# Kernel tuning notes

Measured on AMD Instinct MI355X. Metric: run time of the kernel, lower is better.

## Reference

```python
import jax, jax.numpy as jnp
import numpy as np

N_NODES = 50000
N_COLORS = 256
D = 64
H = 128  # MLP hidden = 2*D
E_VV = 800000
E_VC = 400000


def _mlp_params(key, d_in, d_hid, d_out):
    k1, k2 = jax.random.split(key)
    s1 = 1.0 / np.sqrt(d_in)
    s2 = 1.0 / np.sqrt(d_hid)
    return (
        jax.random.uniform(k1, (d_in, d_hid), jnp.float32, -s1, s1),
        jnp.zeros((d_hid,), jnp.float32),
        jax.random.uniform(k2, (d_hid, d_out), jnp.float32, -s2, s2),
        jnp.zeros((d_out,), jnp.float32),
    )


def setup_inputs() -> dict:
    key = jax.random.key(0)
    ks = jax.random.split(key, 8)
    x_v = jax.random.normal(ks[0], (N_NODES, D), jnp.float32)
    x_c = jax.random.normal(ks[1], (N_COLORS, D), jnp.float32)
    src_vv = jax.random.randint(ks[2], (E_VV,), 0, N_NODES, jnp.int32)
    dst_vv = jax.random.randint(ks[3], (E_VV,), 0, N_NODES, jnp.int32)
    src_vc = jax.random.randint(ks[4], (E_VC,), 0, N_COLORS, jnp.int32)
    dst_vc = jax.random.randint(ks[5], (E_VC,), 0, N_NODES, jnp.int32)
    W1v, b1v, W2v, b2v = _mlp_params(ks[6], D, H, D)
    W1c, b1c, W2c, b2c = _mlp_params(ks[7], D, H, D)
    return {
        "x_v": x_v, "x_c": x_c,
        "W1v": W1v, "b1v": b1v, "W2v": W2v, "b2v": b2v,
        "W1c": W1c, "b1c": b1c, "W2c": W2c, "b2c": b2c,
        "src_vv": src_vv, "dst_vv": dst_vv,
        "src_vc": src_vc, "dst_vc": dst_vc,
    }


def reference(x_v, x_c, W1v, b1v, W2v, b2v, W1c, b1c, W2c, b2c,
              src_vv, dst_vv, src_vc, dst_vc):
    n = x_v.shape[0]
    # vertex->vertex messages: gather, MLP, scatter-sum
    mv = jax.nn.relu(x_v[src_vv] @ W1v + b1v) @ W2v + b2v  # [E_vv, D]
    agg_v = jax.ops.segment_sum(mv, dst_vv, num_segments=n)
    # color->vertex messages: gather color embeddings, MLP, scatter-sum
    mc = jax.nn.relu(x_c[src_vc] @ W1c + b1c) @ W2c + b2c  # [E_vc, D]
    agg_c = jax.ops.segment_sum(mc, dst_vc, num_segments=n)
    return jax.nn.relu(x_v + agg_v + agg_c)
```

## Files before the change

kernel.cpp:

```cpp
#include <hip/hip_runtime.h>

#define NN 50000
#define NC 256
#define DD 64
#define HH 128
#define EVV 800000
#define EVC 400000
#define NE 1200000
#define NB 196
#define BCAP 8192
#define MLPV_B 782
#define MLPC_B 4
#define MLP_B (MLPV_B + MLPC_B)
#define FILL_EPB 2048
#define FILL_B 586
#define QUADS 197
#define K1_B (QUADS * 7)
#define VCAP 64
#define HROW 136

typedef __attribute__((ext_vector_type(8))) short bf16x8;
typedef __attribute__((ext_vector_type(4))) float f32x4;

__device__ __forceinline__ unsigned short f2bf(float x) {
  unsigned u = __float_as_uint(x);
  u = (u + 0x7fffu + ((u >> 16) & 1u)) >> 16;
  return (unsigned short)u;
}

union SMem {
  unsigned short hl[4][16 * HROW];
  struct {
    int cnt[NB];
    int off[NB];
    int gbase[NB];
    int sa[256], sb[256];
    unsigned int stage[FILL_EPB];
  } f;
};

__global__ __launch_bounds__(256) void prep_kernel(
    const float* __restrict__ W1v, const float* __restrict__ W2v,
    const float* __restrict__ W1c, const float* __restrict__ W2c,
    unsigned short* __restrict__ wt, int* __restrict__ gcur) {
  const int tid = blockIdx.x * 256 + threadIdx.x;
  if (tid < NB) gcur[tid] = 0;
  const int sel = tid >> 13;
  const int t = tid & 8191;
  unsigned short* dst = wt + sel * 8192;
  if (sel == 0) {
    const int n = t >> 6, k = t & 63;
    dst[t] = f2bf(W1v[k * HH + n]);
  } else if (sel == 1) {
    const int n = t >> 7, k = t & 127;
    dst[t] = f2bf(W2v[k * DD + n]);
  } else if (sel == 2) {
    const int n = t >> 6, k = t & 63;
    dst[t] = f2bf(W1c[k * HH + n]);
  } else {
    const int n = t >> 7, k = t & 127;
    dst[t] = f2bf(W2c[k * DD + n]);
  }
}

__device__ __forceinline__ void mlp_mfma(
    const float* __restrict__ X, const unsigned short* __restrict__ W1t,
    const float* __restrict__ b1, const unsigned short* __restrict__ W2t,
    const float* __restrict__ b2, unsigned short* __restrict__ Y, int blk,
    int nrows, unsigned short* __restrict__ hl) {
  const int lane = threadIdx.x & 63;
  const int m = lane & 15;
  const int quad = lane >> 4;
  const int rowbase = blk * 64 + (threadIdx.x >> 6) * 16;

  bf16x8 a0, a1;
  {
    float4 xa = {0.f, 0.f, 0.f, 0.f}, xb = xa, xc = xa, xd = xa;
    const int row = rowbase + m;
    if (row < nrows) {
      const float* xp = X + (size_t)row * DD + quad * 8;
      xa = *(const float4*)(xp);
      xb = *(const float4*)(xp + 4);
      xc = *(const float4*)(xp + 32);
      xd = *(const float4*)(xp + 36);
    }
    a0[0] = (short)f2bf(xa.x); a0[1] = (short)f2bf(xa.y);
    a0[2] = (short)f2bf(xa.z); a0[3] = (short)f2bf(xa.w);
    a0[4] = (short)f2bf(xb.x); a0[5] = (short)f2bf(xb.y);
    a0[6] = (short)f2bf(xb.z); a0[7] = (short)f2bf(xb.w);
    a1[0] = (short)f2bf(xc.x); a1[1] = (short)f2bf(xc.y);
    a1[2] = (short)f2bf(xc.z); a1[3] = (short)f2bf(xc.w);
    a1[4] = (short)f2bf(xd.x); a1[5] = (short)f2bf(xd.y);
    a1[6] = (short)f2bf(xd.z); a1[7] = (short)f2bf(xd.w);
  }

#pragma unroll
  for (int nt = 0; nt < 8; ++nt) {
    const int n = nt * 16 + m;
    const float bv = b1[n];
    f32x4 acc = {bv, bv, bv, bv};
    const bf16x8 b0 = *(const bf16x8*)(W1t + n * 64 + quad * 8);
    const bf16x8 b1f = *(const bf16x8*)(W1t + n * 64 + 32 + quad * 8);
    acc = __builtin_amdgcn_mfma_f32_16x16x32_bf16(a0, b0, acc, 0, 0, 0);
    acc = __builtin_amdgcn_mfma_f32_16x16x32_bf16(a1, b1f, acc, 0, 0, 0);
#pragma unroll
    for (int r = 0; r < 4; ++r)
      hl[(quad * 4 + r) * HROW + n] = f2bf(fmaxf(acc[r], 0.f));
  }

  bf16x8 ha[4];
#pragma unroll
  for (int kc = 0; kc < 4; ++kc)
    ha[kc] = *(const bf16x8*)(hl + m * HROW + kc * 32 + quad * 8);

#pragma unroll
  for (int nt = 0; nt < 4; ++nt) {
    const int n = nt * 16 + m;
    const float bv = b2[n];
    f32x4 acc = {bv, bv, bv, bv};
#pragma unroll
    for (int kc = 0; kc < 4; ++kc) {
      const bf16x8 bw = *(const bf16x8*)(W2t + n * 128 + kc * 32 + quad * 8);
      acc = __builtin_amdgcn_mfma_f32_16x16x32_bf16(ha[kc], bw, acc, 0, 0, 0);
    }
#pragma unroll
    for (int r = 0; r < 4; ++r) {
      const int row = rowbase + quad * 4 + r;
      if (row < nrows) Y[(size_t)row * DD + n] = f2bf(acc[r]);
    }
  }
}

__device__ __forceinline__ void fill_block(
    const int* __restrict__ src_vv, const int* __restrict__ dst_vv,
    const int* __restrict__ src_vc, const int* __restrict__ dst_vc,
    int* __restrict__ gcur, unsigned int* __restrict__ records, int blk,
    SMem* sm) {
  const int t = threadIdx.x;
  const int base = blk * FILL_EPB;
  if (t < NB) sm->f.cnt[t] = 0;
  __syncthreads();

  unsigned int rec[8];
  int rk[8];
#pragma unroll
  for (int r = 0; r < 8; ++r) {
    const int e = base + r * 256 + t;
    rk[r] = -1;
    if (e < NE) {
      int s, d;
      if (e < EVV) {
        s = src_vv[e];
        d = dst_vv[e];
      } else {
        s = NN + src_vc[e - EVV];
        d = dst_vc[e - EVV];
      }
      rec[r] = ((unsigned int)d << 16) | (unsigned int)s;
      rk[r] = atomicAdd(&sm->f.cnt[d >> 8], 1);
    }
  }
  __syncthreads();

  const int val = (t < NB) ? sm->f.cnt[t] : 0;
  sm->f.sa[t] = val;
  __syncthreads();
  int* s = sm->f.sa;
  int* d = sm->f.sb;
  for (int o = 1; o < 256; o <<= 1) {
    d[t] = s[t] + ((t >= o) ? s[t - o] : 0);
    __syncthreads();
    int* tmp = s; s = d; d = tmp;
  }
  if (t < NB) {
    sm->f.off[t] = s[t] - val;
    sm->f.gbase[t] = t * BCAP + ((val > 0) ? atomicAdd(&gcur[t], val) : 0);
  }
  __syncthreads();

#pragma unroll
  for (int r = 0; r < 8; ++r)
    if (rk[r] >= 0) sm->f.stage[sm->f.off[rec[r] >> 24] + rk[r]] = rec[r];
  __syncthreads();

  const int total = (NE - base < FILL_EPB) ? (NE - base) : FILL_EPB;
  for (int i = t; i < total; i += 256) {
    const unsigned int u = sm->f.stage[i];
    const int b2 = u >> 24;
    records[sm->f.gbase[b2] + (i - sm->f.off[b2])] = u;
  }
}

__global__ __launch_bounds__(256) void k1_kernel(
    const float* __restrict__ x_v, const float* __restrict__ x_c,
    const float* __restrict__ b1v, const float* __restrict__ b2v,
    const float* __restrict__ b1c, const float* __restrict__ b2c,
    const unsigned short* __restrict__ wt,
    const int* __restrict__ src_vv, const int* __restrict__ dst_vv,
    const int* __restrict__ src_vc, const int* __restrict__ dst_vc,
    unsigned short* __restrict__ table, int* __restrict__ gcur,
    unsigned int* __restrict__ records) {
  __shared__ SMem sm;
  const int q = blockIdx.x / 7;
  const int r = blockIdx.x % 7;
  if (r < 3) {
    const int fid = q * 3 + r;
    if (fid >= FILL_B) return;
    fill_block(src_vv, dst_vv, src_vc, dst_vc, gcur, records, fid, &sm);
  } else {
    const int mb = q * 4 + (r - 3);
    if (mb >= MLP_B) return;
    unsigned short* hl = sm.hl[threadIdx.x >> 6];
    if (mb < MLPV_B)
      mlp_mfma(x_v, wt, b1v, wt + 8192, b2v, table, mb, NN, hl);
    else
      mlp_mfma(x_c, wt + 16384, b1c, wt + 24576, b2c,
               table + (size_t)NN * DD, mb - MLPV_B, NC, hl);
  }
}

__device__ __forceinline__ void acc8(float* a, const uint4 t) {
  a[0] += __uint_as_float(t.x << 16);
  a[1] += __uint_as_float(t.x & 0xffff0000u);
  a[2] += __uint_as_float(t.y << 16);
  a[3] += __uint_as_float(t.y & 0xffff0000u);
  a[4] += __uint_as_float(t.z << 16);
  a[5] += __uint_as_float(t.z & 0xffff0000u);
  a[6] += __uint_as_float(t.w << 16);
  a[7] += __uint_as_float(t.w & 0xffff0000u);
}

__device__ __forceinline__ void place(unsigned int u, int* c1,
                                      unsigned short* slots) {
  const int lv = (u >> 16) & 255;
  const int pos = atomicAdd(&c1[lv], 1);
  if (pos < VCAP) slots[lv * VCAP + pos] = (unsigned short)(u & 0xffffu);
}

__global__ __launch_bounds__(1024) void gather_kernel(
    const uint4* __restrict__ table4, const unsigned int* __restrict__ records,
    const int* __restrict__ gcur, const float4* __restrict__ xv4,
    float4* __restrict__ out4) {
  __shared__ int c1[256];
  __shared__ unsigned short slots[256 * VCAP];
  const int t = threadIdx.x;
  const int bucket = blockIdx.x;
  const int start = bucket * BCAP;
  const int nrec = gcur[bucket];

  if (t < 256) c1[t] = 0;
  __syncthreads();

  const uint4* rec4 = (const uint4*)(records + start);
  const int nfull = nrec >> 2;
  for (int q = t; q < nfull; q += 1024) {
    const uint4 u = rec4[q];
    place(u.x, c1, slots);
    place(u.y, c1, slots);
    place(u.z, c1, slots);
    place(u.w, c1, slots);
  }
  for (int j = (nfull << 2) + t; j < nrec; j += 1024)
    place(records[start + j], c1, slots);
  __syncthreads();

  const int g = t >> 3;
  const int c = t & 7;
  for (int p = 0; p < 2; ++p) {
    const int lv = p * 128 + g;
    const int v = bucket * 256 + lv;
    if (v >= NN) continue;
    const size_t ob = (size_t)v * 16 + c * 2;
    const float4 x0 = xv4[ob];
    const float4 x1 = xv4[ob + 1];
    int n = c1[lv];
    n = (n > VCAP) ? VCAP : n;
    const unsigned short* sl = slots + lv * VCAP;

    float a[8];
#pragma unroll
    for (int r = 0; r < 8; ++r) a[r] = 0.f;

    int i = 0;
    for (; i + 8 <= n; i += 8) {
      const int e0 = sl[i + 0];
      const int e1 = sl[i + 1];
      const int e2 = sl[i + 2];
      const int e3 = sl[i + 3];
      const int e4 = sl[i + 4];
      const int e5 = sl[i + 5];
      const int e6 = sl[i + 6];
      const int e7 = sl[i + 7];
      const uint4 t0 = table4[(size_t)e0 * 8 + c];
      const uint4 t1 = table4[(size_t)e1 * 8 + c];
      const uint4 t2 = table4[(size_t)e2 * 8 + c];
      const uint4 t3 = table4[(size_t)e3 * 8 + c];
      const uint4 t4 = table4[(size_t)e4 * 8 + c];
      const uint4 t5 = table4[(size_t)e5 * 8 + c];
      const uint4 t6 = table4[(size_t)e6 * 8 + c];
      const uint4 t7 = table4[(size_t)e7 * 8 + c];
      acc8(a, t0); acc8(a, t1); acc8(a, t2); acc8(a, t3);
      acc8(a, t4); acc8(a, t5); acc8(a, t6); acc8(a, t7);
    }
    for (; i + 4 <= n; i += 4) {
      const int e0 = sl[i + 0];
      const int e1 = sl[i + 1];
      const int e2 = sl[i + 2];
      const int e3 = sl[i + 3];
      const uint4 t0 = table4[(size_t)e0 * 8 + c];
      const uint4 t1 = table4[(size_t)e1 * 8 + c];
      const uint4 t2 = table4[(size_t)e2 * 8 + c];
      const uint4 t3 = table4[(size_t)e3 * 8 + c];
      acc8(a, t0); acc8(a, t1); acc8(a, t2); acc8(a, t3);
    }
    for (; i < n; ++i) {
      const uint4 t0 = table4[(size_t)sl[i] * 8 + c];
      acc8(a, t0);
    }

    float4 o0, o1;
    o0.x = fmaxf(x0.x + a[0], 0.f);
    o0.y = fmaxf(x0.y + a[1], 0.f);
    o0.z = fmaxf(x0.z + a[2], 0.f);
    o0.w = fmaxf(x0.w + a[3], 0.f);
    o1.x = fmaxf(x1.x + a[4], 0.f);
    o1.y = fmaxf(x1.y + a[5], 0.f);
    o1.z = fmaxf(x1.z + a[6], 0.f);
    o1.w = fmaxf(x1.w + a[7], 0.f);
    out4[ob] = o0;
    out4[ob + 1] = o1;
  }
}

extern "C" void kernel_launch(void* const* d_in, const int* in_sizes, int n_in,
                              void* d_out, int out_size, void* d_ws,
                              size_t ws_size, hipStream_t stream) {
  const float* x_v = (const float*)d_in[0];
  const float* x_c = (const float*)d_in[1];
  const float* W1v = (const float*)d_in[2];
  const float* b1v = (const float*)d_in[3];
  const float* W2v = (const float*)d_in[4];
  const float* b2v = (const float*)d_in[5];
  const float* W1c = (const float*)d_in[6];
  const float* b1c = (const float*)d_in[7];
  const float* W2c = (const float*)d_in[8];
  const float* b2c = (const float*)d_in[9];
  const int* src_vv = (const int*)d_in[10];
  const int* dst_vv = (const int*)d_in[11];
  const int* src_vc = (const int*)d_in[12];
  const int* dst_vc = (const int*)d_in[13];
  float* out = (float*)d_out;

  char* p = (char*)d_ws;
  unsigned short* table = (unsigned short*)p;
  p += (size_t)(NN + NC) * DD * sizeof(unsigned short);
  unsigned int* records = (unsigned int*)p;
  p += (size_t)NB * BCAP * sizeof(unsigned int);
  unsigned short* wt = (unsigned short*)p;
  p += (size_t)4 * 8192 * sizeof(unsigned short);
  int* gcur = (int*)p;

  prep_kernel<<<128, 256, 0, stream>>>(W1v, W2v, W1c, W2c, wt, gcur);

  k1_kernel<<<K1_B, 256, 0, stream>>>(x_v, x_c, b1v, b2v, b1c, b2c, wt,
                                      src_vv, dst_vv, src_vc, dst_vc, table,
                                      gcur, records);

  gather_kernel<<<NB, 1024, 0, stream>>>((const uint4*)table, records, gcur,
                                         (const float4*)x_v, (float4*)out);
}
```

Before: 139.0 us.

## Use 1024-thread k1 blocks, wave-shuffle scan, and split gather buckets in halves

The fused fill/MLP kernel moves to 1024-thread blocks: each fill block handles 8192 edges and each MLP block handles 256 rows, and the block-wide shared-memory prefix scan becomes a single-wave shuffle scan. The gather kernel launches two blocks per bucket. Each block filters the records for its half of the 256 vertices, which doubles the grid and halves shared memory per block, and it loads x_v before the placement phase. The aim is to cut per-block overhead and barrier count and to raise gather occupancy. In exchange, every gather block now reads all records of its bucket, so record reads double, and k1 runs far fewer, larger blocks.

```diff
diff --git a/kernel.cpp b/kernel.cpp
--- a/kernel.cpp
+++ b/kernel.cpp
@@ -9,13 +9,14 @@
 #define NE 1200000
 #define NB 196
 #define BCAP 8192
-#define MLPV_B 782
-#define MLPC_B 4
+#define MLPV_B 196
+#define MLPC_B 1
 #define MLP_B (MLPV_B + MLPC_B)
-#define FILL_EPB 2048
-#define FILL_B 586
-#define QUADS 197
-#define K1_B (QUADS * 7)
+#define FILL_EPB 8192
+#define FILL_B 147
+#define SEPT 50
+#define K1_B (SEPT * 7)
+#define GAT_B (NB * 2)
 #define VCAP 64
 #define HROW 136
 
@@ -29,12 +30,12 @@
 }
 
 union SMem {
-  unsigned short hl[4][16 * HROW];
+  unsigned short hl[16][16 * HROW];
   struct {
     int cnt[NB];
     int off[NB];
     int gbase[NB];
-    int sa[256], sb[256];
+    int sa[256];
     unsigned int stage[FILL_EPB];
   } f;
 };
@@ -71,7 +72,7 @@
   const int lane = threadIdx.x & 63;
   const int m = lane & 15;
   const int quad = lane >> 4;
-  const int rowbase = blk * 64 + (threadIdx.x >> 6) * 16;
+  const int rowbase = blk * 256 + (threadIdx.x >> 6) * 16;
 
   bf16x8 a0, a1;
   {
@@ -145,7 +146,7 @@
   int rk[8];
 #pragma unroll
   for (int r = 0; r < 8; ++r) {
-    const int e = base + r * 256 + t;
+    const int e = base + r * 1024 + t;
     rk[r] = -1;
     if (e < NE) {
       int s, d;
@@ -162,18 +163,26 @@
   }
   __syncthreads();
 
-  const int val = (t < NB) ? sm->f.cnt[t] : 0;
-  sm->f.sa[t] = val;
-  __syncthreads();
-  int* s = sm->f.sa;
-  int* d = sm->f.sb;
-  for (int o = 1; o < 256; o <<= 1) {
-    d[t] = s[t] + ((t >= o) ? s[t - o] : 0);
-    __syncthreads();
-    int* tmp = s; s = d; d = tmp;
-  }
+  if (t < 64) {
+    int carry = 0;
+    for (int ch = 0; ch < 4; ++ch) {
+      const int idx = ch * 64 + t;
+      int v = (idx < NB) ? sm->f.cnt[idx] : 0;
+#pragma unroll
+      for (int o = 1; o < 64; o <<= 1) {
+        const int u = __shfl_up(v, o, 64);
+        if (t >= o) v += u;
+      }
+      const int inc = v + carry;
+      if (idx < NB) sm->f.sa[idx] = inc;
+      carry = __shfl(inc, 63, 64);
+    }
+  }
+  __syncthreads();
+
   if (t < NB) {
-    sm->f.off[t] = s[t] - val;
+    const int val = sm->f.cnt[t];
+    sm->f.off[t] = sm->f.sa[t] - val;
     sm->f.gbase[t] = t * BCAP + ((val > 0) ? atomicAdd(&gcur[t], val) : 0);
   }
   __syncthreads();
@@ -184,14 +193,14 @@
   __syncthreads();
 
   const int total = (NE - base < FILL_EPB) ? (NE - base) : FILL_EPB;
-  for (int i = t; i < total; i += 256) {
+  for (int i = t; i < total; i += 1024) {
     const unsigned int u = sm->f.stage[i];
     const int b2 = u >> 24;
     records[sm->f.gbase[b2] + (i - sm->f.off[b2])] = u;
   }
 }
 
-__global__ __launch_bounds__(256) void k1_kernel(
+__global__ __launch_bounds__(1024) void k1_kernel(
     const float* __restrict__ x_v, const float* __restrict__ x_c,
     const float* __restrict__ b1v, const float* __restrict__ b2v,
     const float* __restrict__ b1c, const float* __restrict__ b2c,
@@ -230,106 +239,111 @@
   a[7] += __uint_as_float(t.w & 0xffff0000u);
 }
 
-__device__ __forceinline__ void place(unsigned int u, int* c1,
-                                      unsigned short* slots) {
-  const int lv = (u >> 16) & 255;
-  const int pos = atomicAdd(&c1[lv], 1);
-  if (pos < VCAP) slots[lv * VCAP + pos] = (unsigned short)(u & 0xffffu);
+__device__ __forceinline__ void place(unsigned int u, unsigned int hsel,
+                                      int* c1, unsigned short* slots) {
+  const unsigned int lv = (u >> 16) & 255u;
+  if ((lv & 128u) == hsel) {
+    const int lg = (int)(lv & 127u);
+    const int pos = atomicAdd(&c1[lg], 1);
+    if (pos < VCAP) slots[lg * VCAP + pos] = (unsigned short)(u & 0xffffu);
+  }
 }
 
 __global__ __launch_bounds__(1024) void gather_kernel(
     const uint4* __restrict__ table4, const unsigned int* __restrict__ records,
     const int* __restrict__ gcur, const float4* __restrict__ xv4,
     float4* __restrict__ out4) {
-  __shared__ int c1[256];
-  __shared__ unsigned short slots[256 * VCAP];
+  __shared__ int c1[128];
+  __shared__ unsigned short slots[128 * VCAP];
   const int t = threadIdx.x;
-  const int bucket = blockIdx.x;
+  const int bucket = blockIdx.x >> 1;
+  const unsigned int hsel = (blockIdx.x & 1) << 7;
   const int start = bucket * BCAP;
   const int nrec = gcur[bucket];
-
-  if (t < 256) c1[t] = 0;
+  const int g = t >> 3;
+  const int c = t & 7;
+  const int v = bucket * 256 + (int)hsel + g;
+  const size_t ob = (size_t)v * 16 + c * 2;
+
+  float4 x0 = {0.f, 0.f, 0.f, 0.f}, x1 = x0;
+  if (v < NN) {
+    x0 = xv4[ob];
+    x1 = xv4[ob + 1];
+  }
+
+  if (t < 128) c1[t] = 0;
   __syncthreads();
 
   const uint4* rec4 = (const uint4*)(records + start);
   const int nfull = nrec >> 2;
   for (int q = t; q < nfull; q += 1024) {
     const uint4 u = rec4[q];
-    place(u.x, c1, slots);
-    place(u.y, c1, slots);
-    place(u.z, c1, slots);
-    place(u.w, c1, slots);
+    place(u.x, hsel, c1, slots);
+    place(u.y, hsel, c1, slots);
+    place(u.z, hsel, c1, slots);
+    place(u.w, hsel, c1, slots);
   }
   for (int j = (nfull << 2) + t; j < nrec; j += 1024)
-    place(records[start + j], c1, slots);
-  __syncthreads();
-
-  const int g = t >> 3;
-  const int c = t & 7;
-  for (int p = 0; p < 2; ++p) {
-    const int lv = p * 128 + g;
-    const int v = bucket * 256 + lv;
-    if (v >= NN) continue;
-    const size_t ob = (size_t)v * 16 + c * 2;
-    const float4 x0 = xv4[ob];
-    const float4 x1 = xv4[ob + 1];
-    int n = c1[lv];
-    n = (n > VCAP) ? VCAP : n;
-    const unsigned short* sl = slots + lv * VCAP;
-
-    float a[8];
-#pragma unroll
-    for (int r = 0; r < 8; ++r) a[r] = 0.f;
-
-    int i = 0;
-    for (; i + 8 <= n; i += 8) {
-      const int e0 = sl[i + 0];
-      const int e1 = sl[i + 1];
-      const int e2 = sl[i + 2];
-      const int e3 = sl[i + 3];
-      const int e4 = sl[i + 4];
-      const int e5 = sl[i + 5];
-      const int e6 = sl[i + 6];
-      const int e7 = sl[i + 7];
-      const uint4 t0 = table4[(size_t)e0 * 8 + c];
-      const uint4 t1 = table4[(size_t)e1 * 8 + c];
-      const uint4 t2 = table4[(size_t)e2 * 8 + c];
-      const uint4 t3 = table4[(size_t)e3 * 8 + c];
-      const uint4 t4 = table4[(size_t)e4 * 8 + c];
-      const uint4 t5 = table4[(size_t)e5 * 8 + c];
-      const uint4 t6 = table4[(size_t)e6 * 8 + c];
-      const uint4 t7 = table4[(size_t)e7 * 8 + c];
-      acc8(a, t0); acc8(a, t1); acc8(a, t2); acc8(a, t3);
-      acc8(a, t4); acc8(a, t5); acc8(a, t6); acc8(a, t7);
-    }
-    for (; i + 4 <= n; i += 4) {
-      const int e0 = sl[i + 0];
-      const int e1 = sl[i + 1];
-      const int e2 = sl[i + 2];
-      const int e3 = sl[i + 3];
-      const uint4 t0 = table4[(size_t)e0 * 8 + c];
-      const uint4 t1 = table4[(size_t)e1 * 8 + c];
-      const uint4 t2 = table4[(size_t)e2 * 8 + c];
-      const uint4 t3 = table4[(size_t)e3 * 8 + c];
-      acc8(a, t0); acc8(a, t1); acc8(a, t2); acc8(a, t3);
-    }
-    for (; i < n; ++i) {
-      const uint4 t0 = table4[(size_t)sl[i] * 8 + c];
-      acc8(a, t0);
-    }
-
-    float4 o0, o1;
-    o0.x = fmaxf(x0.x + a[0], 0.f);
-    o0.y = fmaxf(x0.y + a[1], 0.f);
-    o0.z = fmaxf(x0.z + a[2], 0.f);
-    o0.w = fmaxf(x0.w + a[3], 0.f);
-    o1.x = fmaxf(x1.x + a[4], 0.f);
-    o1.y = fmaxf(x1.y + a[5], 0.f);
-    o1.z = fmaxf(x1.z + a[6], 0.f);
-    o1.w = fmaxf(x1.w + a[7], 0.f);
-    out4[ob] = o0;
-    out4[ob + 1] = o1;
-  }
+    place(records[start + j], hsel, c1, slots);
+  __syncthreads();
+
+  if (v >= NN) return;
+  int n = c1[g];
+  n = (n > VCAP) ? VCAP : n;
+  const unsigned short* sl = slots + g * VCAP;
+
+  float a[8];
+#pragma unroll
+  for (int r = 0; r < 8; ++r) a[r] = 0.f;
+
+  int i = 0;
+  for (; i + 8 <= n; i += 8) {
+    const int e0 = sl[i + 0];
+    const int e1 = sl[i + 1];
+    const int e2 = sl[i + 2];
+    const int e3 = sl[i + 3];
+    const int e4 = sl[i + 4];
+    const int e5 = sl[i + 5];
+    const int e6 = sl[i + 6];
+    const int e7 = sl[i + 7];
+    const uint4 t0 = table4[(size_t)e0 * 8 + c];
+    const uint4 t1 = table4[(size_t)e1 * 8 + c];
+    const uint4 t2 = table4[(size_t)e2 * 8 + c];
+    const uint4 t3 = table4[(size_t)e3 * 8 + c];
+    const uint4 t4 = table4[(size_t)e4 * 8 + c];
+    const uint4 t5 = table4[(size_t)e5 * 8 + c];
+    const uint4 t6 = table4[(size_t)e6 * 8 + c];
+    const uint4 t7 = table4[(size_t)e7 * 8 + c];
+    acc8(a, t0); acc8(a, t1); acc8(a, t2); acc8(a, t3);
+    acc8(a, t4); acc8(a, t5); acc8(a, t6); acc8(a, t7);
+  }
+  for (; i + 4 <= n; i += 4) {
+    const int e0 = sl[i + 0];
+    const int e1 = sl[i + 1];
+    const int e2 = sl[i + 2];
+    const int e3 = sl[i + 3];
+    const uint4 t0 = table4[(size_t)e0 * 8 + c];
+    const uint4 t1 = table4[(size_t)e1 * 8 + c];
+    const uint4 t2 = table4[(size_t)e2 * 8 + c];
+    const uint4 t3 = table4[(size_t)e3 * 8 + c];
+    acc8(a, t0); acc8(a, t1); acc8(a, t2); acc8(a, t3);
+  }
+  for (; i < n; ++i) {
+    const uint4 t0 = table4[(size_t)sl[i] * 8 + c];
+    acc8(a, t0);
+  }
+
+  float4 o0, o1;
+  o0.x = fmaxf(x0.x + a[0], 0.f);
+  o0.y = fmaxf(x0.y + a[1], 0.f);
+  o0.z = fmaxf(x0.z + a[2], 0.f);
+  o0.w = fmaxf(x0.w + a[3], 0.f);
+  o1.x = fmaxf(x1.x + a[4], 0.f);
+  o1.y = fmaxf(x1.y + a[5], 0.f);
+  o1.z = fmaxf(x1.z + a[6], 0.f);
+  o1.w = fmaxf(x1.w + a[7], 0.f);
+  out4[ob] = o0;
+  out4[ob + 1] = o1;
 }
 
 extern "C" void kernel_launch(void* const* d_in, const int* in_sizes, int n_in,
@@ -362,10 +376,10 @@
 
   prep_kernel<<<128, 256, 0, stream>>>(W1v, W2v, W1c, W2c, wt, gcur);
 
-  k1_kernel<<<K1_B, 256, 0, stream>>>(x_v, x_c, b1v, b2v, b1c, b2c, wt,
-                                      src_vv, dst_vv, src_vc, dst_vc, table,
-                                      gcur, records);
-
-  gather_kernel<<<NB, 1024, 0, stream>>>((const uint4*)table, records, gcur,
-                                         (const float4*)x_v, (float4*)out);
-}
+  k1_kernel<<<K1_B, 1024, 0, stream>>>(x_v, x_c, b1v, b2v, b1c, b2c, wt,
+                                       src_vv, dst_vv, src_vc, dst_vc, table,
+                                       gcur, records);
+
+  gather_kernel<<<GAT_B, 1024, 0, stream>>>((const uint4*)table, records, gcur,
+                                            (const float4*)x_v, (float4*)out);
+}
```

New measurement: 137.6 us. No clear change (-1.0%).
